# Performance work log

Measured on AMD Instinct MI355X. Metric: run time of the kernel, lower is better.

The kernel has to match this reference:

```python
import jax, jax.numpy as jnp
import numpy as np


def setup_inputs() -> dict:
    key = jax.random.key(0)
    kq, kk, kv = jax.random.split(key, 3)
    B, S, H, D = 2, 2048, 32, 128
    q = jax.random.normal(kq, (B, S, H, D), dtype=jnp.float32)
    k = jax.random.normal(kk, (B, S, H, D), dtype=jnp.float32)
    v = jax.random.normal(kv, (B, S, H, D), dtype=jnp.float32)
    return {"q": q, "k": k, "v": v}


def _causal_attention(q, k, v):
    # q,k,v: [B, S, H, D] (flash-attn layout). Zigzag ring attention computes
    # exactly standard causal attention; zigzag only balances work across ranks.
    B, S, H, D = q.shape
    scale = 1.0 / jnp.sqrt(jnp.asarray(D, q.dtype))
    scores = jnp.einsum('bqhd,bkhd->bhqk', q, k) * scale  # [B,H,S,S]
    causal = jnp.tril(jnp.ones((S, S), dtype=bool))
    scores = jnp.where(causal, scores, jnp.finfo(scores.dtype).min)
    probs = jax.nn.softmax(scores, axis=-1)
    return jnp.einsum('bhqk,bkhd->bqhd', probs, v)  # [B,S,H,D]


def reference(q, k, v):
    out = _causal_attention(q, k, v)
    return jnp.sum(out)
```

## Files before the change

kernel.cpp:

```cpp
#include <hip/hip_runtime.h>
#include <hip/hip_bf16.h>
#include <stdint.h>

#define B_ 2
#define S_ 2048
#define H_ 32
#define D_ 128
#define R_ (B_*H_*S_)
#define PG 2048
#define CPB 36

typedef __bf16 bf16x8 __attribute__((ext_vector_type(8)));
typedef float  f32x16 __attribute__((ext_vector_type(16)));

#if __has_builtin(__builtin_amdgcn_exp2f)
#define EXP2F(x) __builtin_amdgcn_exp2f(x)
#else
#define EXP2F(x) exp2f(x)
#endif

#define AS1 __attribute__((address_space(1)))
#define AS3 __attribute__((address_space(3)))

__device__ __forceinline__ unsigned short f2bf(float f) {
  unsigned u = __float_as_uint(f);
  u += 0x7FFFu + ((u >> 16) & 1u);
  return (unsigned short)(u >> 16);
}

__device__ __forceinline__ unsigned int cvtpk(float a, float b) {
  unsigned int r;
  asm("v_cvt_pk_bf16_f32 %0, %1, %2" : "=v"(r) : "v"(a), "v"(b));
  return r;
}

__global__ __launch_bounds__(256) void prep(
    const float* __restrict__ kf, const float* __restrict__ v,
    unsigned short* __restrict__ kc,
    float* __restrict__ vsum, float* __restrict__ nd, float* __restrict__ out0) {
  const int bid = blockIdx.x;
  const int t = threadIdx.x;
  if (bid == 0 && t == 0) out0[0] = 0.f;

  #pragma unroll
  for (int g = 0; g < 4; ++g) {
    const size_t i = (size_t)g * (PG * 256) + (size_t)bid * 256 + t;
    const float4 a = *reinterpret_cast<const float4*>(kf + i * 8);
    const float4 b = *reinterpret_cast<const float4*>(kf + i * 8 + 4);
    union { unsigned short u[8]; uint4 v4; } o;
    o.u[0] = f2bf(a.x); o.u[1] = f2bf(a.y);
    o.u[2] = f2bf(a.z); o.u[3] = f2bf(a.w);
    o.u[4] = f2bf(b.x); o.u[5] = f2bf(b.y);
    o.u[6] = f2bf(b.z); o.u[7] = f2bf(b.w);
    *reinterpret_cast<uint4*>(kc + i * 8) = o.v4;
  }

  #pragma unroll
  for (int g = 0; g < (B_ * S_) / PG; ++g) {
    const int u = bid + g * PG;
    const int b = u / S_, s = u % S_;
    const float4* panel =
        reinterpret_cast<const float4*>(v + (((size_t)b * S_ + s) * H_) * D_);
    #pragma unroll
    for (int j = 0; j < 4; ++j) {
      const float4 a = panel[j * 256 + t];
      float sum = a.x + a.y + a.z + a.w;
      sum += __shfl_xor(sum, 1);
      sum += __shfl_xor(sum, 2);
      sum += __shfl_xor(sum, 4);
      sum += __shfl_xor(sum, 8);
      sum += __shfl_xor(sum, 16);
      const int h = j * 8 + (t >> 5);
      if ((t & 31) == 0) vsum[((size_t)b * H_ + h) * S_ + s] = sum;
    }
  }

  if (bid < 256) {
    float4* p = reinterpret_cast<float4*>(nd);
    p[(size_t)bid * 256 + t] = float4{0.f, 0.f, 0.f, 0.f};
  }
}

__global__ __launch_bounds__(256, 3) void attn_sum(
    const float* __restrict__ qf, const unsigned short* __restrict__ kc,
    const float* __restrict__ vsum, float* __restrict__ numb,
    float* __restrict__ denb) {
  __shared__ uint4 kbuf[3][512];
  __shared__ float vsbuf[3][64];

  const int id = blockIdx.x;
  const int y  = id >> 3;
  const int bh = (id & 7) + 8 * (y / CPB);
  const int c  = y % CPB;

  int g, h;
  if (c < 1)       { g = 0; h = c;      }
  else if (c < 3)  { g = 1; h = c - 1;  }
  else if (c < 6)  { g = 2; h = c - 3;  }
  else if (c < 10) { g = 3; h = c - 6;  }
  else if (c < 15) { g = 4; h = c - 10; }
  else if (c < 21) { g = 5; h = c - 15; }
  else if (c < 28) { g = 6; h = c - 21; }
  else             { g = 7; h = c - 28; }
  const int st0 = 8 * h, st1 = st0 + 8;

  const int t  = threadIdx.x;
  const int w  = t >> 6;
  const int l  = t & 63;
  const int ln = l & 31, l5 = l >> 5;

  const int b0 = bh >> 5, h0 = bh & 31;
  const int qminA = (2 * g) * 128 + w * 32;
  const int qminB = (2 * g + 1) * 128 + w * 32;
  const unsigned short* kc0 = kc + ((size_t)b0 * S_ * H_ + h0) * D_;
  const float* vsrc0 = vsum + (size_t)bh * S_;

  const float sc = 0.0883883476483184f * 1.4426950408889634f;
  bf16x8 qfA[8], qfB[8];
  {
    const float* qpA = qf + (((size_t)b0 * S_ + qminA + ln) * H_ + h0) * D_ + l5 * 8;
    const float* qpB = qf + (((size_t)b0 * S_ + qminB + ln) * H_ + h0) * D_ + l5 * 8;
    #pragma unroll
    for (int kb8 = 0; kb8 < 8; ++kb8) {
      float4 a = *reinterpret_cast<const float4*>(qpA + kb8 * 16);
      float4 b = *reinterpret_cast<const float4*>(qpA + kb8 * 16 + 4);
      union { unsigned int u[4]; bf16x8 v; } oA;
      oA.u[0] = cvtpk(a.x * sc, a.y * sc); oA.u[1] = cvtpk(a.z * sc, a.w * sc);
      oA.u[2] = cvtpk(b.x * sc, b.y * sc); oA.u[3] = cvtpk(b.z * sc, b.w * sc);
      qfA[kb8] = oA.v;
      a = *reinterpret_cast<const float4*>(qpB + kb8 * 16);
      b = *reinterpret_cast<const float4*>(qpB + kb8 * 16 + 4);
      union { unsigned int u[4]; bf16x8 v; } oB;
      oB.u[0] = cvtpk(a.x * sc, a.y * sc); oB.u[1] = cvtpk(a.z * sc, a.w * sc);
      oB.u[2] = cvtpk(b.x * sc, b.y * sc); oB.u[3] = cvtpk(b.z * sc, b.w * sc);
      qfB[kb8] = oB.v;
    }
  }

  auto stage = [&](int st, int slot) {
    #pragma unroll
    for (int j = 0; j < 2; ++j) {
      const int idx = (w * 2 + j) * 64 + l;
      const int r   = idx >> 4;
      const int p   = idx & 15;
      const int cc  = p ^ (r & 15);
      const unsigned short* src = kc0 + (size_t)(st * 32 + r) * (H_ * D_) + cc * 8;
      __builtin_amdgcn_global_load_lds(
          (const AS1 void*)src, (AS3 void*)(&kbuf[slot][idx & ~63]), 16, 0, 0);
    }
    __builtin_amdgcn_global_load_lds(
        (const AS1 void*)(vsrc0 + st * 32 + l), (AS3 void*)(&vsbuf[slot][0]), 4, 0, 0);
  };

  float npA = 0.f, dpA = 0.f, npB = 0.f, dpB = 0.f;

  stage(st0, st0 % 3);
  stage(st0 + 1, (st0 + 1) % 3);

  const int xr = ln & 15;
  for (int st = st0; st < st1; ++st) {
    if (st + 1 < st1) asm volatile("s_waitcnt vmcnt(3)" ::: "memory");
    else              asm volatile("s_waitcnt vmcnt(0)" ::: "memory");
    __builtin_amdgcn_s_barrier();
    if (st + 2 < st1) stage(st + 2, (st + 2) % 3);

    const int kbase = st * 32;
    if (kbase <= qminB + 31) {
      const int slot = st % 3;
      const uint4* rowb = &kbuf[slot][ln * 16];
      bf16x8 kfr[8];
      #pragma unroll
      for (int kb8 = 0; kb8 < 8; ++kb8)
        kfr[kb8] = *reinterpret_cast<const bf16x8*>(&rowb[(kb8 * 2 + l5) ^ xr]);
      const float4 vs0 = *reinterpret_cast<const float4*>(&vsbuf[slot][ 0 + 4 * l5]);
      const float4 vs1 = *reinterpret_cast<const float4*>(&vsbuf[slot][ 8 + 4 * l5]);
      const float4 vs2 = *reinterpret_cast<const float4*>(&vsbuf[slot][16 + 4 * l5]);
      const float4 vs3 = *reinterpret_cast<const float4*>(&vsbuf[slot][24 + 4 * l5]);
      const float vsa[16] = {vs0.x,vs0.y,vs0.z,vs0.w, vs1.x,vs1.y,vs1.z,vs1.w,
                             vs2.x,vs2.y,vs2.z,vs2.w, vs3.x,vs3.y,vs3.z,vs3.w};

      {
        f32x16 sacc = {0.f,0.f,0.f,0.f,0.f,0.f,0.f,0.f,
                       0.f,0.f,0.f,0.f,0.f,0.f,0.f,0.f};
        __builtin_amdgcn_s_setprio(1);
        #pragma unroll
        for (int kb8 = 0; kb8 < 8; ++kb8)
          sacc = __builtin_amdgcn_mfma_f32_32x32x16_bf16(kfr[kb8], qfB[kb8], sacc, 0, 0, 0);
        __builtin_amdgcn_s_setprio(0);
        if (kbase + 31 <= qminB) {
          #pragma unroll
          for (int r = 0; r < 16; ++r) {
            const float e = EXP2F(sacc[r]);
            dpB += e;
            npB = fmaf(e, vsa[r], npB);
          }
        } else {
          const int qg = qminB + ln;
          #pragma unroll
          for (int r = 0; r < 16; ++r) {
            const int kr = kbase + (r & 3) + 8 * (r >> 2) + 4 * l5;
            const float e = (kr <= qg) ? EXP2F(sacc[r]) : 0.f;
            dpB += e;
            npB = fmaf(e, vsa[r], npB);
          }
        }
      }
      if (kbase <= qminA + 31) {
        f32x16 sacc = {0.f,0.f,0.f,0.f,0.f,0.f,0.f,0.f,
                       0.f,0.f,0.f,0.f,0.f,0.f,0.f,0.f};
        __builtin_amdgcn_s_setprio(1);
        #pragma unroll
        for (int kb8 = 0; kb8 < 8; ++kb8)
          sacc = __builtin_amdgcn_mfma_f32_32x32x16_bf16(kfr[kb8], qfA[kb8], sacc, 0, 0, 0);
        __builtin_amdgcn_s_setprio(0);
        if (kbase + 31 <= qminA) {
          #pragma unroll
          for (int r = 0; r < 16; ++r) {
            const float e = EXP2F(sacc[r]);
            dpA += e;
            npA = fmaf(e, vsa[r], npA);
          }
        } else {
          const int qg = qminA + ln;
          #pragma unroll
          for (int r = 0; r < 16; ++r) {
            const int kr = kbase + (r & 3) + 8 * (r >> 2) + 4 * l5;
            const float e = (kr <= qg) ? EXP2F(sacc[r]) : 0.f;
            dpA += e;
            npA = fmaf(e, vsa[r], npA);
          }
        }
      }
    }
  }

  npA += __shfl_xor(npA, 32); dpA += __shfl_xor(dpA, 32);
  npB += __shfl_xor(npB, 32); dpB += __shfl_xor(dpB, 32);
  if (l5 == 0) {
    float* nrow = numb + (size_t)bh * S_;
    float* drow = denb + (size_t)bh * S_;
    atomicAdd(&nrow[qminA + ln], npA);
    atomicAdd(&drow[qminA + ln], dpA);
    atomicAdd(&nrow[qminB + ln], npB);
    atomicAdd(&drow[qminB + ln], dpB);
  }
}

__global__ __launch_bounds__(256) void finalize(
    const float* __restrict__ numb, const float* __restrict__ denb,
    float* __restrict__ out) {
  const int i = blockIdx.x * 256 + threadIdx.x;
  float c = numb[i] / denb[i];
  #pragma unroll
  for (int m = 1; m < 64; m <<= 1) c += __shfl_xor(c, m);
  __shared__ float ps[4];
  if ((threadIdx.x & 63) == 0) ps[threadIdx.x >> 6] = c;
  __syncthreads();
  if (threadIdx.x == 0) atomicAdd(out, ps[0] + ps[1] + ps[2] + ps[3]);
}

extern "C" void kernel_launch(void* const* d_in, const int* in_sizes, int n_in,
                              void* d_out, int out_size, void* d_ws, size_t ws_size,
                              hipStream_t stream) {
  const float* q = (const float*)d_in[0];
  const float* k = (const float*)d_in[1];
  const float* v = (const float*)d_in[2];
  float* out = (float*)d_out;

  unsigned short* kc = (unsigned short*)d_ws;
  float* vsum = (float*)(kc + (size_t)R_ * D_);
  float* numb = vsum + R_;
  float* denb = numb + R_;

  hipLaunchKernelGGL(prep, dim3(PG), dim3(256), 0, stream,
                     k, v, kc, vsum, numb, out);
  hipLaunchKernelGGL(attn_sum, dim3(64 * CPB), dim3(256), 0, stream,
                     q, kc, vsum, numb, denb);
  hipLaunchKernelGGL(finalize, dim3(R_ / 256), dim3(256), 0, stream,
                     numb, denb, out);
}
```

Measured before the change: 108.0 us.

## Switch attention-sum to single-wave blocks with flattened triangular work partition

Replaces 4-wave blocks that each handled a fixed pair of 128-row query groups with single-wave (64-thread) blocks. Each block processes exactly 8 (query-64-row, key-32-tile) units from a flattened enumeration of the causal triangle, and flushes partial sums with atomics whenever the query tile changes. The intent is to balance work evenly and drop the workgroup barrier, using a double-buffered LDS stage. In exchange, K tiles are no longer shared across 4 waves, so global/LDS load traffic per MFMA rises, and there are more atomics and more Q reloads.

```diff
diff --git a/kernel.cpp b/kernel.cpp
--- a/kernel.cpp
+++ b/kernel.cpp
@@ -8,7 +8,7 @@
 #define D_ 128
 #define R_ (B_*H_*S_)
 #define PG 2048
-#define CPB 36
+#define CPB 132
 
 typedef __bf16 bf16x8 __attribute__((ext_vector_type(8)));
 typedef float  f32x16 __attribute__((ext_vector_type(16)));
@@ -81,45 +81,52 @@
   }
 }
 
-__global__ __launch_bounds__(256, 3) void attn_sum(
+__global__ __launch_bounds__(64, 4) void attn_sum(
     const float* __restrict__ qf, const unsigned short* __restrict__ kc,
     const float* __restrict__ vsum, float* __restrict__ numb,
     float* __restrict__ denb) {
-  __shared__ uint4 kbuf[3][512];
-  __shared__ float vsbuf[3][64];
+  __shared__ uint4 kbuf[2][512];
+  __shared__ float vsbuf[2][64];
 
   const int id = blockIdx.x;
   const int y  = id >> 3;
   const int bh = (id & 7) + 8 * (y / CPB);
   const int c  = y % CPB;
 
-  int g, h;
-  if (c < 1)       { g = 0; h = c;      }
-  else if (c < 3)  { g = 1; h = c - 1;  }
-  else if (c < 6)  { g = 2; h = c - 3;  }
-  else if (c < 10) { g = 3; h = c - 6;  }
-  else if (c < 15) { g = 4; h = c - 10; }
-  else if (c < 21) { g = 5; h = c - 15; }
-  else if (c < 28) { g = 6; h = c - 21; }
-  else             { g = 7; h = c - 28; }
-  const int st0 = 8 * h, st1 = st0 + 8;
-
-  const int t  = threadIdx.x;
-  const int w  = t >> 6;
-  const int l  = t & 63;
+  const int l  = threadIdx.x;
   const int ln = l & 31, l5 = l >> 5;
 
   const int b0 = bh >> 5, h0 = bh & 31;
-  const int qminA = (2 * g) * 128 + w * 32;
-  const int qminB = (2 * g + 1) * 128 + w * 32;
   const unsigned short* kc0 = kc + ((size_t)b0 * S_ * H_ + h0) * D_;
   const float* vsrc0 = vsum + (size_t)bh * S_;
+  float* nrow = numb + (size_t)bh * S_;
+  float* drow = denb + (size_t)bh * S_;
+
+  const int f0 = c * 8, fend = f0 + 8;
+  int j = 0;
+  while ((j + 1) * (j + 2) <= f0) ++j;
+  int st = f0 - j * (j + 1);
+
+  auto stage = [&](int stk, int slot) {
+    #pragma unroll
+    for (int i = 0; i < 8; ++i) {
+      const int idx = i * 64 + l;
+      const int r   = idx >> 4;
+      const int p   = idx & 15;
+      const int cc  = p ^ (r & 15);
+      const unsigned short* src = kc0 + (size_t)(stk * 32 + r) * (H_ * D_) + cc * 8;
+      __builtin_amdgcn_global_load_lds(
+          (const AS1 void*)src, (AS3 void*)(&kbuf[slot][idx & ~63]), 16, 0, 0);
+    }
+    __builtin_amdgcn_global_load_lds(
+        (const AS1 void*)(vsrc0 + stk * 32 + l), (AS3 void*)(&vsbuf[slot][0]), 4, 0, 0);
+  };
 
   const float sc = 0.0883883476483184f * 1.4426950408889634f;
   bf16x8 qfA[8], qfB[8];
-  {
-    const float* qpA = qf + (((size_t)b0 * S_ + qminA + ln) * H_ + h0) * D_ + l5 * 8;
-    const float* qpB = qf + (((size_t)b0 * S_ + qminB + ln) * H_ + h0) * D_ + l5 * 8;
+  auto loadQ = [&](int jq) {
+    const float* qpA = qf + (((size_t)b0 * S_ + jq * 64 + ln) * H_ + h0) * D_ + l5 * 8;
+    const float* qpB = qpA + (size_t)32 * (H_ * D_);
     #pragma unroll
     for (int kb8 = 0; kb8 < 8; ++kb8) {
       float4 a = *reinterpret_cast<const float4*>(qpA + kb8 * 16);
@@ -135,115 +142,107 @@
       oB.u[2] = cvtpk(b.x * sc, b.y * sc); oB.u[3] = cvtpk(b.z * sc, b.w * sc);
       qfB[kb8] = oB.v;
     }
-  }
-
-  auto stage = [&](int st, int slot) {
-    #pragma unroll
-    for (int j = 0; j < 2; ++j) {
-      const int idx = (w * 2 + j) * 64 + l;
-      const int r   = idx >> 4;
-      const int p   = idx & 15;
-      const int cc  = p ^ (r & 15);
-      const unsigned short* src = kc0 + (size_t)(st * 32 + r) * (H_ * D_) + cc * 8;
-      __builtin_amdgcn_global_load_lds(
-          (const AS1 void*)src, (AS3 void*)(&kbuf[slot][idx & ~63]), 16, 0, 0);
-    }
-    __builtin_amdgcn_global_load_lds(
-        (const AS1 void*)(vsrc0 + st * 32 + l), (AS3 void*)(&vsbuf[slot][0]), 4, 0, 0);
   };
 
   float npA = 0.f, dpA = 0.f, npB = 0.f, dpB = 0.f;
-
-  stage(st0, st0 % 3);
-  stage(st0 + 1, (st0 + 1) % 3);
+  auto flush = [&](int jq) {
+    npA += __shfl_xor(npA, 32); dpA += __shfl_xor(dpA, 32);
+    npB += __shfl_xor(npB, 32); dpB += __shfl_xor(dpB, 32);
+    if (l5 == 0) {
+      atomicAdd(&nrow[jq * 64 + ln], npA);
+      atomicAdd(&drow[jq * 64 + ln], dpA);
+      atomicAdd(&nrow[jq * 64 + 32 + ln], npB);
+      atomicAdd(&drow[jq * 64 + 32 + ln], dpB);
+    }
+    npA = dpA = npB = dpB = 0.f;
+  };
+
+  int fs = f0, js = j, sts = st;
+  auto advS = [&]() { ++fs; ++sts; if (sts == 2 * js + 2) { sts = 0; ++js; } };
+
+  stage(sts, fs & 1); advS();
+  if (fs < fend) { stage(sts, fs & 1); advS(); }
+
+  int jq = j;
+  loadQ(jq);
 
   const int xr = ln & 15;
-  for (int st = st0; st < st1; ++st) {
-    if (st + 1 < st1) asm volatile("s_waitcnt vmcnt(3)" ::: "memory");
+  for (int f = f0; f < fend; ++f) {
+    if (j != jq) { flush(jq); jq = j; loadQ(jq); }
+
+    if (f + 1 < fend) asm volatile("s_waitcnt vmcnt(9)" ::: "memory");
     else              asm volatile("s_waitcnt vmcnt(0)" ::: "memory");
-    __builtin_amdgcn_s_barrier();
-    if (st + 2 < st1) stage(st + 2, (st + 2) % 3);
+
+    const int slot = f & 1;
+    const uint4* rowb = &kbuf[slot][ln * 16];
+    bf16x8 kfr[8];
+    #pragma unroll
+    for (int kb8 = 0; kb8 < 8; ++kb8)
+      kfr[kb8] = *reinterpret_cast<const bf16x8*>(&rowb[(kb8 * 2 + l5) ^ xr]);
+    const float4 vs0 = *reinterpret_cast<const float4*>(&vsbuf[slot][ 0 + 4 * l5]);
+    const float4 vs1 = *reinterpret_cast<const float4*>(&vsbuf[slot][ 8 + 4 * l5]);
+    const float4 vs2 = *reinterpret_cast<const float4*>(&vsbuf[slot][16 + 4 * l5]);
+    const float4 vs3 = *reinterpret_cast<const float4*>(&vsbuf[slot][24 + 4 * l5]);
+    const float vsa[16] = {vs0.x,vs0.y,vs0.z,vs0.w, vs1.x,vs1.y,vs1.z,vs1.w,
+                           vs2.x,vs2.y,vs2.z,vs2.w, vs3.x,vs3.y,vs3.z,vs3.w};
+    asm volatile("s_waitcnt lgkmcnt(0)" ::: "memory");
+    __builtin_amdgcn_sched_barrier(0);
+    if (fs < fend) { stage(sts, fs & 1); advS(); }
 
     const int kbase = st * 32;
-    if (kbase <= qminB + 31) {
-      const int slot = st % 3;
-      const uint4* rowb = &kbuf[slot][ln * 16];
-      bf16x8 kfr[8];
+    if (st <= 2 * j) {
+      f32x16 sacc = {0.f,0.f,0.f,0.f,0.f,0.f,0.f,0.f,
+                     0.f,0.f,0.f,0.f,0.f,0.f,0.f,0.f};
+      __builtin_amdgcn_s_setprio(1);
       #pragma unroll
       for (int kb8 = 0; kb8 < 8; ++kb8)
-        kfr[kb8] = *reinterpret_cast<const bf16x8*>(&rowb[(kb8 * 2 + l5) ^ xr]);
-      const float4 vs0 = *reinterpret_cast<const float4*>(&vsbuf[slot][ 0 + 4 * l5]);
-      const float4 vs1 = *reinterpret_cast<const float4*>(&vsbuf[slot][ 8 + 4 * l5]);
-      const float4 vs2 = *reinterpret_cast<const float4*>(&vsbuf[slot][16 + 4 * l5]);
-      const float4 vs3 = *reinterpret_cast<const float4*>(&vsbuf[slot][24 + 4 * l5]);
-      const float vsa[16] = {vs0.x,vs0.y,vs0.z,vs0.w, vs1.x,vs1.y,vs1.z,vs1.w,
-                             vs2.x,vs2.y,vs2.z,vs2.w, vs3.x,vs3.y,vs3.z,vs3.w};
-
-      {
-        f32x16 sacc = {0.f,0.f,0.f,0.f,0.f,0.f,0.f,0.f,
-                       0.f,0.f,0.f,0.f,0.f,0.f,0.f,0.f};
-        __builtin_amdgcn_s_setprio(1);
-        #pragma unroll
-        for (int kb8 = 0; kb8 < 8; ++kb8)
-          sacc = __builtin_amdgcn_mfma_f32_32x32x16_bf16(kfr[kb8], qfB[kb8], sacc, 0, 0, 0);
-        __builtin_amdgcn_s_setprio(0);
-        if (kbase + 31 <= qminB) {
-          #pragma unroll
-          for (int r = 0; r < 16; ++r) {
-            const float e = EXP2F(sacc[r]);
-            dpB += e;
-            npB = fmaf(e, vsa[r], npB);
-          }
-        } else {
-          const int qg = qminB + ln;
-          #pragma unroll
-          for (int r = 0; r < 16; ++r) {
-            const int kr = kbase + (r & 3) + 8 * (r >> 2) + 4 * l5;
-            const float e = (kr <= qg) ? EXP2F(sacc[r]) : 0.f;
-            dpB += e;
-            npB = fmaf(e, vsa[r], npB);
-          }
+        sacc = __builtin_amdgcn_mfma_f32_32x32x16_bf16(kfr[kb8], qfA[kb8], sacc, 0, 0, 0);
+      __builtin_amdgcn_s_setprio(0);
+      if (st < 2 * j) {
+        #pragma unroll
+        for (int r = 0; r < 16; ++r) {
+          const float e = EXP2F(sacc[r]);
+          dpA += e; npA = fmaf(e, vsa[r], npA);
+        }
+      } else {
+        const int qg = j * 64 + ln;
+        #pragma unroll
+        for (int r = 0; r < 16; ++r) {
+          const int kr = kbase + (r & 3) + 8 * (r >> 2) + 4 * l5;
+          const float e = (kr <= qg) ? EXP2F(sacc[r]) : 0.f;
+          dpA += e; npA = fmaf(e, vsa[r], npA);
         }
       }
-      if (kbase <= qminA + 31) {
-        f32x16 sacc = {0.f,0.f,0.f,0.f,0.f,0.f,0.f,0.f,
-                       0.f,0.f,0.f,0.f,0.f,0.f,0.f,0.f};
-        __builtin_amdgcn_s_setprio(1);
-        #pragma unroll
-        for (int kb8 = 0; kb8 < 8; ++kb8)
-          sacc = __builtin_amdgcn_mfma_f32_32x32x16_bf16(kfr[kb8], qfA[kb8], sacc, 0, 0, 0);
-        __builtin_amdgcn_s_setprio(0);
-        if (kbase + 31 <= qminA) {
-          #pragma unroll
-          for (int r = 0; r < 16; ++r) {
-            const float e = EXP2F(sacc[r]);
-            dpA += e;
-            npA = fmaf(e, vsa[r], npA);
-          }
-        } else {
-          const int qg = qminA + ln;
-          #pragma unroll
-          for (int r = 0; r < 16; ++r) {
-            const int kr = kbase + (r & 3) + 8 * (r >> 2) + 4 * l5;
-            const float e = (kr <= qg) ? EXP2F(sacc[r]) : 0.f;
-            dpA += e;
-            npA = fmaf(e, vsa[r], npA);
-          }
+    }
+    {
+      f32x16 sacc = {0.f,0.f,0.f,0.f,0.f,0.f,0.f,0.f,
+                     0.f,0.f,0.f,0.f,0.f,0.f,0.f,0.f};
+      __builtin_amdgcn_s_setprio(1);
+      #pragma unroll
+      for (int kb8 = 0; kb8 < 8; ++kb8)
+        sacc = __builtin_amdgcn_mfma_f32_32x32x16_bf16(kfr[kb8], qfB[kb8], sacc, 0, 0, 0);
+      __builtin_amdgcn_s_setprio(0);
+      if (st < 2 * j + 1) {
+        #pragma unroll
+        for (int r = 0; r < 16; ++r) {
+          const float e = EXP2F(sacc[r]);
+          dpB += e; npB = fmaf(e, vsa[r], npB);
+        }
+      } else {
+        const int qg = j * 64 + 32 + ln;
+        #pragma unroll
+        for (int r = 0; r < 16; ++r) {
+          const int kr = kbase + (r & 3) + 8 * (r >> 2) + 4 * l5;
+          const float e = (kr <= qg) ? EXP2F(sacc[r]) : 0.f;
+          dpB += e; npB = fmaf(e, vsa[r], npB);
         }
       }
     }
-  }
-
-  npA += __shfl_xor(npA, 32); dpA += __shfl_xor(dpA, 32);
-  npB += __shfl_xor(npB, 32); dpB += __shfl_xor(dpB, 32);
-  if (l5 == 0) {
-    float* nrow = numb + (size_t)bh * S_;
-    float* drow = denb + (size_t)bh * S_;
-    atomicAdd(&nrow[qminA + ln], npA);
-    atomicAdd(&drow[qminA + ln], dpA);
-    atomicAdd(&nrow[qminB + ln], npB);
-    atomicAdd(&drow[qminB + ln], dpB);
-  }
+
+    ++st;
+    if (st == 2 * j + 2) { st = 0; ++j; }
+  }
+  flush(jq);
 }
 
 __global__ __launch_bounds__(256) void finalize(
@@ -274,7 +273,7 @@
 
   hipLaunchKernelGGL(prep, dim3(PG), dim3(256), 0, stream,
                      k, v, kc, vsum, numb, out);
-  hipLaunchKernelGGL(attn_sum, dim3(64 * CPB), dim3(256), 0, stream,
+  hipLaunchKernelGGL(attn_sum, dim3(64 * CPB * 8 / 8), dim3(64), 0, stream,
                      q, kc, vsum, numb, denb);
   hipLaunchKernelGGL(finalize, dim3(R_ / 256), dim3(256), 0, stream,
                      numb, denb, out);
```

New measurement: 113.2 us. 4.8% more time.
